# Optimization experiments

Measured on AMD Instinct MI355X. Metric: run time of the kernel, lower is better.

## Reference

```python
import jax, jax.numpy as jnp
import numpy as np

N_ATOMS = 100000
N_EDGES = 6400000
CUTOFF = 12.0
CUTOFF_SR = 2.0
CUTOFF_SQ = CUTOFF * CUTOFF
KEHALF = 7.199822675975274  # ASE kehalf, unit factors = 1


def poly6_switch(d, cutoff):
    # Poly6 smooth switch-off: 1 at d=0, 0 at d>=cutoff
    x = d / cutoff
    sw = 1.0 - 10.0 * x**3 + 15.0 * x**4 - 6.0 * x**5
    return jnp.where(d < cutoff, sw, jnp.zeros_like(sw))


def setup_inputs() -> dict:
    key = jax.random.key(0)
    k1, k2, k3, k4, k5 = jax.random.split(key, 5)
    atomic_charges = jax.random.normal(k1, (N_ATOMS,), dtype=jnp.float32) * 0.3
    atomic_dipoles = jax.random.normal(k2, (N_ATOMS,), dtype=jnp.float32) * 0.1
    # distances in (0.5, 13.5): some pairs inside short-range, some beyond cutoff
    distances = jax.random.uniform(k3, (N_EDGES,), dtype=jnp.float32) * 13.0 + 0.5
    idx_i = jax.random.randint(k4, (N_EDGES,), 0, N_ATOMS, dtype=jnp.int32)
    idx_j = jax.random.randint(k5, (N_EDGES,), 0, N_ATOMS, dtype=jnp.int32)
    return {
        "atomic_charges": atomic_charges,
        "atomic_dipoles": atomic_dipoles,
        "distances": distances,
        "idx_i": idx_i,
        "idx_j": idx_j,
    }


def reference(atomic_charges, atomic_dipoles, distances, idx_i, idx_j):
    # gather per-edge charges / dipoles
    qi = atomic_charges[idx_i]
    qj = atomic_charges[idx_j]
    di = atomic_dipoles[idx_i]
    dj = atomic_dipoles[idx_j]

    d = distances
    d_sh = jnp.sqrt(d * d + 1.0)  # shielded distance

    sw_off = poly6_switch(d, CUTOFF_SR)
    sw_on = 1.0 - sw_off

    # split_distance=True branch (cutoff != cutoff_short_range):
    # shifted-force Coulomb (charge-charge, ~1/d)
    E_ord_q = 1.0 / d + d / CUTOFF_SQ - 2.0 / CUTOFF
    E_sh_q = 1.0 / d_sh + d_sh / CUTOFF_SQ - 2.0 / CUTOFF
    E_q = KEHALF * qi * qj * (sw_off * E_sh_q + sw_on * E_ord_q)

    # dipole-dipole term (~1/d^3), same shielded/ordinary blending
    E_ord_d = 1.0 / d**3
    E_sh_d = 1.0 / d_sh**3
    E_d = KEHALF * di * dj * (sw_off * E_sh_d + sw_on * E_ord_d)

    E = E_q + E_d
    E = jnp.where(d <= CUTOFF, E, jnp.zeros_like(E))

    # scatter-sum per-edge energies to atoms
    return jax.ops.segment_sum(E, idx_i, num_segments=N_ATOMS)
```

## Files before the change

### kernel.cpp

```cpp
#include <hip/hip_runtime.h>
#include <hip/hip_bf16.h>
#include <hip/hip_fp16.h>

#define CUTOFF_C    12.0f
#define CUTOFF_SR_C 2.0f
#define CUTOFF_SQ_C 144.0f
#define KEHALF_C    7.199822675975274f

__device__ __forceinline__ float edge_energy(float d, float qi, float qj,
                                             float di, float dj) {
    float inv_d   = __frcp_rn(d);
    float dsh     = __fsqrt_rn(fmaf(d, d, 1.0f));
    float inv_dsh = __frcp_rn(dsh);
    float x  = d * (1.0f / CUTOFF_SR_C);
    float x3 = x * x * x;
    float sw = fmaf(x3, fmaf(x, fmaf(x, -6.0f, 15.0f), -10.0f), 1.0f);
    float sw_off = (d < CUTOFF_SR_C) ? sw : 0.0f;
    float Eoq = inv_d   + fmaf(d,   (1.0f / CUTOFF_SQ_C), -(2.0f / CUTOFF_C));
    float Esq = inv_dsh + fmaf(dsh, (1.0f / CUTOFF_SQ_C), -(2.0f / CUTOFF_C));
    float Eq  = (KEHALF_C * qi * qj) * fmaf(sw_off, Esq - Eoq, Eoq);
    float Eod = inv_d * inv_d * inv_d;
    float Esd = inv_dsh * inv_dsh * inv_dsh;
    float Ed  = (KEHALF_C * di * dj) * fmaf(sw_off, Esd - Eod, Eod);
    return Eq + Ed;
}

__global__ __launch_bounds__(256) void pc_pack_qd_h(
    const float* __restrict__ q,
    const float* __restrict__ dip,
    __half2*     __restrict__ qd,
    int n_atoms)
{
    int a = blockIdx.x * 256 + threadIdx.x;
    if (a < n_atoms) qd[a] = __floats2half2_rn(q[a], dip[a]);
}

__device__ __forceinline__ unsigned vw_pack(float d, __half2 hqdj) {
    if (!(d <= CUTOFF_C)) return 0u;
    float2 qdj   = __half22float2(hqdj);
    float inv_d   = __frcp_rn(d);
    float dsh     = __fsqrt_rn(fmaf(d, d, 1.0f));
    float inv_dsh = __frcp_rn(dsh);
    float x  = d * (1.0f / CUTOFF_SR_C);
    float x3 = x * x * x;
    float sw = fmaf(x3, fmaf(x, fmaf(x, -6.0f, 15.0f), -10.0f), 1.0f);
    float sw_off = (d < CUTOFF_SR_C) ? sw : 0.0f;
    float Foq = inv_d   + fmaf(d,   (1.0f / CUTOFF_SQ_C), -(2.0f / CUTOFF_C));
    float Fsq = inv_dsh + fmaf(dsh, (1.0f / CUTOFF_SQ_C), -(2.0f / CUTOFF_C));
    float F   = fmaf(sw_off, Fsq - Foq, Foq);
    float God = inv_d * inv_d * inv_d;
    float Gsd = inv_dsh * inv_dsh * inv_dsh;
    float G   = fmaf(sw_off, Gsd - God, God);
    __half2 r = __floats2half2_rn(KEHALF_C * qdj.x * F, KEHALF_C * qdj.y * G);
    union { __half2 h; unsigned u; } cvt;
    cvt.h = r;
    return cvt.u;
}

__global__ __launch_bounds__(256) void pc_compute_vw(
    const __half2* __restrict__ qd,
    const float*   __restrict__ dist,
    const int*     __restrict__ idx_j,
    unsigned*      __restrict__ vw,
    int n_edges, int n4)
{
    int t = blockIdx.x * 256 + threadIdx.x;
    if (t < n4) {
        int4 j4 = ((const int4*)idx_j)[t];
        __half2 h0 = qd[j4.x];
        __half2 h1 = qd[j4.y];
        __half2 h2 = qd[j4.z];
        __half2 h3 = qd[j4.w];
        float4 d4 = ((const float4*)dist)[t];
        uint4 o;
        o.x = vw_pack(d4.x, h0);
        o.y = vw_pack(d4.y, h1);
        o.z = vw_pack(d4.z, h2);
        o.w = vw_pack(d4.w, h3);
        ((uint4*)vw)[t] = o;
    }
    int total = gridDim.x * 256;
    for (int e = (n4 << 2) + t; e < n_edges; e += total) {
        float d = dist[e];
        vw[e] = (d <= CUTOFF_C) ? vw_pack(d, qd[idx_j[e]]) : 0u;
    }
}

template <int CH, int BLK>
__global__ __launch_bounds__(BLK) void pc_scatter_g(
    const int*      __restrict__ idx_i,
    const unsigned* __restrict__ vw,
    const __half2*  __restrict__ qd,
    float*          __restrict__ partial,
    int n_edges, int n4, int S, int gps, int n_atoms, int nch)
{
    extern __shared__ float acc[];

    const int c    = blockIdx.x % nch;
    const int s    = blockIdx.x / nch;
    const int base = c * CH;
    const int lim  = min(CH, n_atoms - base);

    for (int i = threadIdx.x; i < CH; i += BLK) acc[i] = 0.0f;
    __syncthreads();

    const int g0 = s * gps;
    const int g1 = min(g0 + gps, n4);
    const int4*  idxi4 = (const int4*)idx_i;
    const uint4* vw4   = (const uint4*)vw;

    const __half2 hzero = __floats2half2_rn(0.0f, 0.0f);

    for (int g = g0 + (int)threadIdx.x; g < g1; g += BLK) {
        int4  i4 = idxi4[g];
        uint4 u4 = vw4[g];

        int      ii[4] = { i4.x, i4.y, i4.z, i4.w };
        unsigned uu[4] = { u4.x, u4.y, u4.z, u4.w };
        unsigned lc[4];
        bool     vl[4];
        __half2  qh[4];

        #pragma unroll
        for (int k = 0; k < 4; ++k) {
            lc[k] = (unsigned)(ii[k] - base);
            vl[k] = (lc[k] < (unsigned)CH) && (uu[k] != 0u);
        }
        #pragma unroll
        for (int k = 0; k < 4; ++k)
            qh[k] = vl[k] ? qd[ii[k]] : hzero;
        #pragma unroll
        for (int k = 0; k < 4; ++k) {
            if (vl[k]) {
                union { unsigned u; __half2 h; } cvt; cvt.u = uu[k];
                float2 vf = __half22float2(cvt.h);
                float2 qi = __half22float2(qh[k]);
                atomicAdd(&acc[lc[k]], fmaf(qi.x, vf.x, qi.y * vf.y));
            }
        }
    }

    if (s == S - 1) {
        for (int e = (n4 << 2) + (int)threadIdx.x; e < n_edges; e += BLK) {
            int i = idx_i[e];
            unsigned local = (unsigned)(i - base);
            unsigned u = vw[e];
            if (local < (unsigned)CH && u != 0u) {
                union { unsigned uu; __half2 h; } cvt; cvt.uu = u;
                float2 vf = __half22float2(cvt.h);
                float2 qi = __half22float2(qd[i]);
                atomicAdd(&acc[local], fmaf(qi.x, vf.x, qi.y * vf.y));
            }
        }
    }

    __syncthreads();
    float* row = partial + (size_t)s * n_atoms + base;
    for (int i = threadIdx.x; i < lim; i += BLK) row[i] = acc[i];
}

__global__ __launch_bounds__(256) void pc_reduce(
    const float* __restrict__ partial,
    float*       __restrict__ out,
    int n_atoms, int S)
{
    __shared__ float sh[256];
    int a0   = blockIdx.x * 64;
    int lane = threadIdx.x & 63;
    int w    = threadIdx.x >> 6;
    int a    = a0 + lane;

    float v0 = 0.0f, v1 = 0.0f;
    if (a < n_atoms) {
        int per = S >> 2;
        const float* p = partial + a;
        int s = w * per, send = s + per;
        for (; s + 2 <= send; s += 2) {
            v0 += p[(size_t)(s + 0) * n_atoms];
            v1 += p[(size_t)(s + 1) * n_atoms];
        }
        for (; s < send; ++s) v0 += p[(size_t)s * n_atoms];
    }
    sh[threadIdx.x] = v0 + v1;
    __syncthreads();
    if (w == 0 && a < n_atoms)
        out[a] = (sh[lane] + sh[64 + lane]) + (sh[128 + lane] + sh[192 + lane]);
}

__global__ __launch_bounds__(256) void pc_dipole_edges_atomic(
    const float* __restrict__ q,
    const float* __restrict__ dip,
    const float* __restrict__ dist,
    const int*   __restrict__ idx_i,
    const int*   __restrict__ idx_j,
    float*       __restrict__ out,
    int n_edges)
{
    int t = blockIdx.x * blockDim.x + threadIdx.x;
    const int stride = gridDim.x * blockDim.x;
    for (int e = t; e < n_edges; e += stride) {
        float d = dist[e];
        if (d > CUTOFF_C) continue;
        int i = idx_i[e], j = idx_j[e];
        atomicAdd(&out[i], edge_energy(d, q[i], q[j], dip[i], dip[j]));
    }
}

#define CH_T0 33792
#define CH_T1 20480
#define CH_T2 16384

static bool probe_lds(const void* f, int blk, size_t lds) {
    hipError_t e1 = hipFuncSetAttribute(
        f, hipFuncAttributeMaxDynamicSharedMemorySize, (int)lds);
    int nb = 0;
    hipError_t e2 = hipOccupancyMaxActiveBlocksPerMultiprocessor(&nb, f, blk, lds);
    return (e1 == hipSuccess && e2 == hipSuccess && nb >= 1);
}

extern "C" void kernel_launch(void* const* d_in, const int* in_sizes, int n_in,
                              void* d_out, int out_size, void* d_ws, size_t ws_size,
                              hipStream_t stream) {
    const float* q     = (const float*)d_in[0];
    const float* dip   = (const float*)d_in[1];
    const float* dist  = (const float*)d_in[2];
    const int*   idx_i = (const int*)d_in[3];
    const int*   idx_j = (const int*)d_in[4];
    float*       out   = (float*)d_out;

    int n_edges = in_sizes[2];
    int n_atoms = out_size;
    int n4      = n_edges >> 2;

    int tier, CH, BLK, S;
    size_t lds;
    if (probe_lds((const void*)&pc_scatter_g<CH_T0, 1024>, 1024,
                  (size_t)CH_T0 * 4)) {
        tier = 0; CH = CH_T0; BLK = 1024; S = 84;  lds = (size_t)CH_T0 * 4;
    } else if (probe_lds((const void*)&pc_scatter_g<CH_T1, 512>, 512,
                         (size_t)CH_T1 * 4)) {
        tier = 1; CH = CH_T1; BLK = 512;  S = 100; lds = (size_t)CH_T1 * 4;
    } else {
        tier = 2; CH = CH_T2; BLK = 512;  S = 72;  lds = (size_t)CH_T2 * 4;
    }
    int nch = (n_atoms + CH - 1) / CH;

    size_t qd_b = ((size_t)n_atoms * sizeof(__half2)  + 255) & ~(size_t)255;
    size_t vw_b = ((size_t)n_edges * sizeof(unsigned) + 255) & ~(size_t)255;
    size_t head = qd_b + vw_b;
    size_t avail = (ws_size > head) ? ws_size - head : 0;
    int S_fit = (int)(avail / ((size_t)n_atoms * sizeof(float)));
    if (S_fit < S) S = S_fit & ~3;

    if (S >= 8 && n_atoms > 0) {
        __half2*  qd      = (__half2*)d_ws;
        unsigned* vw      = (unsigned*)((char*)d_ws + qd_b);
        float*    partial = (float*)((char*)d_ws + head);
        int       gps     = (n4 + S - 1) / S;

        pc_pack_qd_h<<<(n_atoms + 255) / 256, 256, 0, stream>>>(q, dip, qd,
                                                                n_atoms);
        int grid1 = (n4 + 255) / 256;
        if (grid1 < 1) grid1 = 1;
        pc_compute_vw<<<grid1, 256, 0, stream>>>(qd, dist, idx_j, vw,
                                                 n_edges, n4);
        if (tier == 0)
            pc_scatter_g<CH_T0, 1024><<<S * nch, 1024, lds, stream>>>(
                idx_i, vw, qd, partial, n_edges, n4, S, gps, n_atoms, nch);
        else if (tier == 1)
            pc_scatter_g<CH_T1, 512><<<S * nch, 512, lds, stream>>>(
                idx_i, vw, qd, partial, n_edges, n4, S, gps, n_atoms, nch);
        else
            pc_scatter_g<CH_T2, 512><<<S * nch, 512, lds, stream>>>(
                idx_i, vw, qd, partial, n_edges, n4, S, gps, n_atoms, nch);
        pc_reduce<<<(n_atoms + 63) / 64, 256, 0, stream>>>(partial, out,
                                                           n_atoms, S);
    } else {
        hipMemsetAsync(out, 0, (size_t)n_atoms * sizeof(float), stream);
        int grid = (n_edges + 255) / 256;
        pc_dipole_edges_atomic<<<grid, 256, 0, stream>>>(
            q, dip, dist, idx_i, idx_j, out, n_edges);
    }
}
```

Before: 183.0 us.

## Fuse per-edge term into scatter and accumulate packed half2 partials per atom

Drops the separate per-edge vw kernel and its intermediate buffer. The scatter kernel now reads distances and idx_j itself, gathers q_j and dipole_j, and computes the switched Coulomb and dipole factors inline. Instead of multiplying by q_i and dip_i per edge, it accumulates the two factors as a half2 in LDS. The reduce kernel multiplies by q_i and dip_i once per atom. Partials are stored in fp16, which halves workspace and reduce traffic but accumulates in half precision and re-reads idx_j and distance for every atom chunk.

```diff
diff --git a/kernel.cpp b/kernel.cpp
--- a/kernel.cpp
+++ b/kernel.cpp
@@ -25,19 +25,8 @@
     return Eq + Ed;
 }
 
-__global__ __launch_bounds__(256) void pc_pack_qd_h(
-    const float* __restrict__ q,
-    const float* __restrict__ dip,
-    __half2*     __restrict__ qd,
-    int n_atoms)
-{
-    int a = blockIdx.x * 256 + threadIdx.x;
-    if (a < n_atoms) qd[a] = __floats2half2_rn(q[a], dip[a]);
-}
-
-__device__ __forceinline__ unsigned vw_pack(float d, __half2 hqdj) {
-    if (!(d <= CUTOFF_C)) return 0u;
-    float2 qdj   = __half22float2(hqdj);
+__device__ __forceinline__ __half2 vw_make(float d, __half2 hqdj) {
+    float2 qdj    = __half22float2(hqdj);
     float inv_d   = __frcp_rn(d);
     float dsh     = __fsqrt_rn(fmaf(d, d, 1.0f));
     float inv_dsh = __frcp_rn(dsh);
@@ -51,72 +40,75 @@
     float God = inv_d * inv_d * inv_d;
     float Gsd = inv_dsh * inv_dsh * inv_dsh;
     float G   = fmaf(sw_off, Gsd - God, God);
-    __half2 r = __floats2half2_rn(KEHALF_C * qdj.x * F, KEHALF_C * qdj.y * G);
-    union { __half2 h; unsigned u; } cvt;
-    cvt.h = r;
-    return cvt.u;
-}
-
-__global__ __launch_bounds__(256) void pc_compute_vw(
+    return __floats2half2_rn(KEHALF_C * qdj.x * F, KEHALF_C * qdj.y * G);
+}
+
+__device__ __forceinline__ unsigned h2bits(__half2 h) {
+    union { __half2 h; unsigned u; } c; c.h = h; return c.u;
+}
+__device__ __forceinline__ __half2 bits2h(unsigned u) {
+    union { unsigned u; __half2 h; } c; c.u = u; return c.h;
+}
+template <typename T>
+__device__ __forceinline__ auto atom_add_h2(T* p, T v, int)
+    -> decltype(atomicAdd(p, v), void()) {
+    atomicAdd(p, v);
+}
+template <typename T>
+__device__ __forceinline__ void atom_add_h2(T* p, T v, long) {
+    unsigned* u = (unsigned*)p;
+    unsigned old = *u, assumed;
+    do {
+        assumed = old;
+        __half2 sum = __hadd2(bits2h(assumed), v);
+        old = atomicCAS(u, assumed, h2bits(sum));
+    } while (old != assumed);
+}
+
+__global__ __launch_bounds__(256) void pc_pack_qd_h(
+    const float* __restrict__ q,
+    const float* __restrict__ dip,
+    __half2*     __restrict__ qd,
+    int n_atoms)
+{
+    int a = blockIdx.x * 256 + threadIdx.x;
+    if (a < n_atoms) qd[a] = __floats2half2_rn(q[a], dip[a]);
+}
+
+template <int CH, int BLK>
+__global__ __launch_bounds__(BLK) void pc_scatter_fused(
+    const float*   __restrict__ dist,
+    const int*     __restrict__ idx_i,
+    const int*     __restrict__ idx_j,
     const __half2* __restrict__ qd,
-    const float*   __restrict__ dist,
-    const int*     __restrict__ idx_j,
-    unsigned*      __restrict__ vw,
-    int n_edges, int n4)
-{
-    int t = blockIdx.x * 256 + threadIdx.x;
-    if (t < n4) {
-        int4 j4 = ((const int4*)idx_j)[t];
-        __half2 h0 = qd[j4.x];
-        __half2 h1 = qd[j4.y];
-        __half2 h2 = qd[j4.z];
-        __half2 h3 = qd[j4.w];
-        float4 d4 = ((const float4*)dist)[t];
-        uint4 o;
-        o.x = vw_pack(d4.x, h0);
-        o.y = vw_pack(d4.y, h1);
-        o.z = vw_pack(d4.z, h2);
-        o.w = vw_pack(d4.w, h3);
-        ((uint4*)vw)[t] = o;
-    }
-    int total = gridDim.x * 256;
-    for (int e = (n4 << 2) + t; e < n_edges; e += total) {
-        float d = dist[e];
-        vw[e] = (d <= CUTOFF_C) ? vw_pack(d, qd[idx_j[e]]) : 0u;
-    }
-}
-
-template <int CH, int BLK>
-__global__ __launch_bounds__(BLK) void pc_scatter_g(
-    const int*      __restrict__ idx_i,
-    const unsigned* __restrict__ vw,
-    const __half2*  __restrict__ qd,
-    float*          __restrict__ partial,
+    __half2*       __restrict__ partial,
     int n_edges, int n4, int S, int gps, int n_atoms, int nch)
 {
-    extern __shared__ float acc[];
+    extern __shared__ __half2 acc2[];
 
     const int c    = blockIdx.x % nch;
     const int s    = blockIdx.x / nch;
     const int base = c * CH;
     const int lim  = min(CH, n_atoms - base);
 
-    for (int i = threadIdx.x; i < CH; i += BLK) acc[i] = 0.0f;
+    const __half2 hzero = __floats2half2_rn(0.0f, 0.0f);
+    for (int i = threadIdx.x; i < CH; i += BLK) acc2[i] = hzero;
     __syncthreads();
 
     const int g0 = s * gps;
     const int g1 = min(g0 + gps, n4);
-    const int4*  idxi4 = (const int4*)idx_i;
-    const uint4* vw4   = (const uint4*)vw;
-
-    const __half2 hzero = __floats2half2_rn(0.0f, 0.0f);
+    const int4*   idxi4 = (const int4*)idx_i;
+    const int4*   idxj4 = (const int4*)idx_j;
+    const float4* dist4 = (const float4*)dist;
 
     for (int g = g0 + (int)threadIdx.x; g < g1; g += BLK) {
-        int4  i4 = idxi4[g];
-        uint4 u4 = vw4[g];
+        int4   i4 = idxi4[g];
+        int4   j4 = idxj4[g];
+        float4 d4 = dist4[g];
 
         int      ii[4] = { i4.x, i4.y, i4.z, i4.w };
-        unsigned uu[4] = { u4.x, u4.y, u4.z, u4.w };
+        int      jj[4] = { j4.x, j4.y, j4.z, j4.w };
+        float    dd[4] = { d4.x, d4.y, d4.z, d4.w };
         unsigned lc[4];
         bool     vl[4];
         __half2  qh[4];
@@ -124,18 +116,16 @@
         #pragma unroll
         for (int k = 0; k < 4; ++k) {
             lc[k] = (unsigned)(ii[k] - base);
-            vl[k] = (lc[k] < (unsigned)CH) && (uu[k] != 0u);
+            vl[k] = (lc[k] < (unsigned)CH) && (dd[k] <= CUTOFF_C);
         }
         #pragma unroll
         for (int k = 0; k < 4; ++k)
-            qh[k] = vl[k] ? qd[ii[k]] : hzero;
+            qh[k] = vl[k] ? qd[jj[k]] : hzero;
         #pragma unroll
         for (int k = 0; k < 4; ++k) {
             if (vl[k]) {
-                union { unsigned u; __half2 h; } cvt; cvt.u = uu[k];
-                float2 vf = __half22float2(cvt.h);
-                float2 qi = __half22float2(qh[k]);
-                atomicAdd(&acc[lc[k]], fmaf(qi.x, vf.x, qi.y * vf.y));
+                __half2 vw = vw_make(dd[k], qh[k]);
+                atom_add_h2(&acc2[lc[k]], vw, 0);
             }
         }
     }
@@ -143,48 +133,52 @@
     if (s == S - 1) {
         for (int e = (n4 << 2) + (int)threadIdx.x; e < n_edges; e += BLK) {
             int i = idx_i[e];
+            float d = dist[e];
             unsigned local = (unsigned)(i - base);
-            unsigned u = vw[e];
-            if (local < (unsigned)CH && u != 0u) {
-                union { unsigned uu; __half2 h; } cvt; cvt.uu = u;
-                float2 vf = __half22float2(cvt.h);
-                float2 qi = __half22float2(qd[i]);
-                atomicAdd(&acc[local], fmaf(qi.x, vf.x, qi.y * vf.y));
+            if (local < (unsigned)CH && d <= CUTOFF_C) {
+                __half2 vw = vw_make(d, qd[idx_j[e]]);
+                atom_add_h2(&acc2[local], vw, 0);
             }
         }
     }
 
     __syncthreads();
-    float* row = partial + (size_t)s * n_atoms + base;
-    for (int i = threadIdx.x; i < lim; i += BLK) row[i] = acc[i];
-}
-
-__global__ __launch_bounds__(256) void pc_reduce(
-    const float* __restrict__ partial,
-    float*       __restrict__ out,
+    __half2* row = partial + (size_t)s * n_atoms + base;
+    for (int i = threadIdx.x; i < lim; i += BLK) row[i] = acc2[i];
+}
+
+__global__ __launch_bounds__(256) void pc_reduce_vw(
+    const __half2* __restrict__ partial,
+    const float*   __restrict__ q,
+    const float*   __restrict__ dip,
+    float*         __restrict__ out,
     int n_atoms, int S)
 {
-    __shared__ float sh[256];
+    __shared__ float2 sh[256];
     int a0   = blockIdx.x * 64;
     int lane = threadIdx.x & 63;
     int w    = threadIdx.x >> 6;
     int a    = a0 + lane;
 
-    float v0 = 0.0f, v1 = 0.0f;
+    float sv = 0.0f, sw = 0.0f;
     if (a < n_atoms) {
         int per = S >> 2;
-        const float* p = partial + a;
+        const __half2* p = partial + a;
         int s = w * per, send = s + per;
-        for (; s + 2 <= send; s += 2) {
-            v0 += p[(size_t)(s + 0) * n_atoms];
-            v1 += p[(size_t)(s + 1) * n_atoms];
-        }
-        for (; s < send; ++s) v0 += p[(size_t)s * n_atoms];
-    }
-    sh[threadIdx.x] = v0 + v1;
+        for (; s < send; ++s) {
+            float2 t = __half22float2(p[(size_t)s * n_atoms]);
+            sv += t.x; sw += t.y;
+        }
+    }
+    sh[threadIdx.x] = make_float2(sv, sw);
     __syncthreads();
-    if (w == 0 && a < n_atoms)
-        out[a] = (sh[lane] + sh[64 + lane]) + (sh[128 + lane] + sh[192 + lane]);
+    if (w == 0 && a < n_atoms) {
+        float2 t0 = sh[lane],       t1 = sh[64 + lane];
+        float2 t2 = sh[128 + lane], t3 = sh[192 + lane];
+        float fv = (t0.x + t1.x) + (t2.x + t3.x);
+        float fw = (t0.y + t1.y) + (t2.y + t3.y);
+        out[a] = fmaf(q[a], fv, dip[a] * fw);
+    }
 }
 
 __global__ __launch_bounds__(256) void pc_dipole_edges_atomic(
@@ -208,7 +202,6 @@
 
 #define CH_T0 33792
 #define CH_T1 20480
-#define CH_T2 16384
 
 static bool probe_lds(const void* f, int blk, size_t lds) {
     hipError_t e1 = hipFuncSetAttribute(
@@ -234,47 +227,36 @@
 
     int tier, CH, BLK, S;
     size_t lds;
-    if (probe_lds((const void*)&pc_scatter_g<CH_T0, 1024>, 1024,
+    if (probe_lds((const void*)&pc_scatter_fused<CH_T0, 1024>, 1024,
                   (size_t)CH_T0 * 4)) {
-        tier = 0; CH = CH_T0; BLK = 1024; S = 84;  lds = (size_t)CH_T0 * 4;
-    } else if (probe_lds((const void*)&pc_scatter_g<CH_T1, 512>, 512,
-                         (size_t)CH_T1 * 4)) {
-        tier = 1; CH = CH_T1; BLK = 512;  S = 100; lds = (size_t)CH_T1 * 4;
+        tier = 0; CH = CH_T0; BLK = 1024; S = 84; lds = (size_t)CH_T0 * 4;
     } else {
-        tier = 2; CH = CH_T2; BLK = 512;  S = 72;  lds = (size_t)CH_T2 * 4;
+        tier = 1; CH = CH_T1; BLK = 512;  S = 48; lds = (size_t)CH_T1 * 4;
     }
     int nch = (n_atoms + CH - 1) / CH;
 
-    size_t qd_b = ((size_t)n_atoms * sizeof(__half2)  + 255) & ~(size_t)255;
-    size_t vw_b = ((size_t)n_edges * sizeof(unsigned) + 255) & ~(size_t)255;
-    size_t head = qd_b + vw_b;
-    size_t avail = (ws_size > head) ? ws_size - head : 0;
-    int S_fit = (int)(avail / ((size_t)n_atoms * sizeof(float)));
+    size_t qd_b  = ((size_t)n_atoms * sizeof(__half2) + 255) & ~(size_t)255;
+    size_t avail = (ws_size > qd_b) ? ws_size - qd_b : 0;
+    int S_fit = (int)(avail / ((size_t)n_atoms * sizeof(__half2)));
     if (S_fit < S) S = S_fit & ~3;
 
     if (S >= 8 && n_atoms > 0) {
-        __half2*  qd      = (__half2*)d_ws;
-        unsigned* vw      = (unsigned*)((char*)d_ws + qd_b);
-        float*    partial = (float*)((char*)d_ws + head);
-        int       gps     = (n4 + S - 1) / S;
+        __half2* qd      = (__half2*)d_ws;
+        __half2* partial = (__half2*)((char*)d_ws + qd_b);
+        int      gps     = (n4 + S - 1) / S;
 
         pc_pack_qd_h<<<(n_atoms + 255) / 256, 256, 0, stream>>>(q, dip, qd,
                                                                 n_atoms);
-        int grid1 = (n4 + 255) / 256;
-        if (grid1 < 1) grid1 = 1;
-        pc_compute_vw<<<grid1, 256, 0, stream>>>(qd, dist, idx_j, vw,
-                                                 n_edges, n4);
         if (tier == 0)
-            pc_scatter_g<CH_T0, 1024><<<S * nch, 1024, lds, stream>>>(
-                idx_i, vw, qd, partial, n_edges, n4, S, gps, n_atoms, nch);
-        else if (tier == 1)
-            pc_scatter_g<CH_T1, 512><<<S * nch, 512, lds, stream>>>(
-                idx_i, vw, qd, partial, n_edges, n4, S, gps, n_atoms, nch);
+            pc_scatter_fused<CH_T0, 1024><<<S * nch, 1024, lds, stream>>>(
+                dist, idx_i, idx_j, qd, partial, n_edges, n4, S, gps,
+                n_atoms, nch);
         else
-            pc_scatter_g<CH_T2, 512><<<S * nch, 512, lds, stream>>>(
-                idx_i, vw, qd, partial, n_edges, n4, S, gps, n_atoms, nch);
-        pc_reduce<<<(n_atoms + 63) / 64, 256, 0, stream>>>(partial, out,
-                                                           n_atoms, S);
+            pc_scatter_fused<CH_T1, 512><<<S * nch, 512, lds, stream>>>(
+                dist, idx_i, idx_j, qd, partial, n_edges, n4, S, gps,
+                n_atoms, nch);
+        pc_reduce_vw<<<(n_atoms + 63) / 64, 256, 0, stream>>>(
+            partial, q, dip, out, n_atoms, S);
     } else {
         hipMemsetAsync(out, 0, (size_t)n_atoms * sizeof(float), stream);
         int grid = (n_edges + 255) / 256;
```

Measured after the change: 165.8 us. 1.1x faster.
